# Optimization experiments

Measured on AMD Instinct MI355X. Metric: run time of the kernel, lower is better.

The kernel has to match this reference:

```python
import jax, jax.numpy as jnp
import numpy as np

B, A, D, H = 2048, 16, 128, 512

def setup_inputs() -> dict:
    key = jax.random.key(0)
    k0, k1, k2, k3, k4 = jax.random.split(key, 5)
    s1 = 1.0 / np.sqrt(D)
    s2 = 1.0 / np.sqrt(H)
    return {
        "attribute_embeddings": jax.random.normal(k0, (B, A, D), dtype=jnp.float32),
        "W1": jax.random.uniform(k1, (H, D), jnp.float32, -s1, s1),  # torch Linear weight [out,in]
        "b1": jax.random.uniform(k2, (H,), jnp.float32, -s1, s1),
        "W2": jax.random.uniform(k3, (D, H), jnp.float32, -s2, s2),
        "b2": jax.random.uniform(k4, (D,), jnp.float32, -s2, s2),
    }

def reference(attribute_embeddings, W1, b1, W2, b2):
    x = attribute_embeddings  # [B, A, D]
    # all pairwise elementwise products: [B, A, A, D]
    pairs = x[:, :, None, :] * x[:, None, :, :]
    # shared 2-layer MLP applied to every pair (torch Linear: y = x @ W.T + b)
    h = jax.nn.relu(jnp.einsum("bijd,hd->bijh", pairs, W1) + b1)
    inter = jnp.einsum("bijh,dh->bijd", h, W2) + b2  # [B, A, A, D]
    # sum over first attribute index i -> [B, A, D]
    return jnp.sum(inter, axis=1)
```

## Files before the change

kernel.cpp:

```cpp
#include <hip/hip_runtime.h>


#define BATCH 2048
#define AA 16
#define DD 128
#define HH 512

typedef __bf16 bf16;
typedef bf16  bf16x4 __attribute__((ext_vector_type(4)));
typedef bf16  bf16x8 __attribute__((ext_vector_type(8)));
typedef float f32x4  __attribute__((ext_vector_type(4)));

__device__ inline f32x4 splat4(float v) { f32x4 r = {v, v, v, v}; return r; }

__global__ __launch_bounds__(256, 1)
void convert_weights(const float* __restrict__ W1,
                     const float* __restrict__ W2,
                     bf16* __restrict__ wsb)
{
    int t = blockIdx.x * 256 + threadIdx.x;
    f32x4 v = (t < 16384) ? *(const f32x4*)(W1 + 4 * t)
                          : *(const f32x4*)(W2 + 4 * (t - 16384));
    bf16x4 o;
    o[0] = (bf16)v[0]; o[1] = (bf16)v[1]; o[2] = (bf16)v[2]; o[3] = (bf16)v[3];
    *(bf16x4*)(wsb + 4 * t) = o;
}

__global__ __launch_bounds__(512, 4)
void interact_kernel(const float* __restrict__ x,
                     const bf16*  __restrict__ W1b,
                     const float* __restrict__ b1,
                     const bf16*  __restrict__ W2b,
                     const float* __restrict__ b2,
                     float* __restrict__ out)
{
    __shared__ float xs[16][136];
    __shared__ __align__(16) unsigned char smem_raw[16 * 16 * 136 * 2];
    bf16 (*ps)[16][136] = reinterpret_cast<bf16(*)[16][136]>(smem_raw);
    bf16 (*hs)[520]     = reinterpret_cast<bf16(*)[520]>(smem_raw);

    const int b    = blockIdx.x;
    const int tid  = threadIdx.x;
    const int wave = tid >> 6;
    const int lane = tid & 63;
    const int quad = lane >> 4;
    const int col  = lane & 15;

    const int jrow = tid >> 5;
    const int dq   = (tid & 31) * 4;

    f32x4 xj;
    {
        const float* src = x + (size_t)b * (AA * DD) + jrow * DD + dq;
        xj = *(const f32x4*)src;
        *(f32x4*)(&xs[jrow][dq]) = xj;
    }

    bf16x8 w1f[4][4];
    f32x4  bias4[4];
#pragma unroll
    for (int n = 0; n < 4; ++n) {
        int h   = wave * 64 + n * 16 + col;
        bias4[n] = splat4(b1[h]);
#pragma unroll
        for (int kk = 0; kk < 4; ++kk)
            w1f[n][kk] = *(const bf16x8*)(W1b + h * DD + kk * 32 + quad * 8);
    }

    f32x4 hsum[4];
#pragma unroll
    for (int n = 0; n < 4; ++n) hsum[n] = splat4(0.f);

    __syncthreads();

#pragma unroll 4
    for (int i = 0; i < 16; ++i) {
        f32x4 xi = *(f32x4*)(&xs[i][dq]);
        bf16x4 pr;
#pragma unroll
        for (int e = 0; e < 4; ++e) pr[e] = (bf16)(xj[e] * xi[e]);
        *(bf16x4*)(&ps[i][jrow][dq]) = pr;
    }
    __syncthreads();

    const int i0 = wave * 2;
#pragma unroll 1
    for (int t = 0; t < 16; ++t) {
        const int i = (i0 + t) & 15;

        bf16x8 af[4];
#pragma unroll
        for (int kk = 0; kk < 4; ++kk)
            af[kk] = *(bf16x8*)(&ps[i][col][kk * 32 + quad * 8]);

        __builtin_amdgcn_s_setprio(1);
        f32x4 acc[4];
#pragma unroll
        for (int n = 0; n < 4; ++n)
            acc[n] = __builtin_amdgcn_mfma_f32_16x16x32_bf16(
                af[0], w1f[n][0], bias4[n], 0, 0, 0);
#pragma unroll
        for (int kk = 1; kk < 4; ++kk)
#pragma unroll
            for (int n = 0; n < 4; ++n)
                acc[n] = __builtin_amdgcn_mfma_f32_16x16x32_bf16(
                    af[kk], w1f[n][kk], acc[n], 0, 0, 0);
        __builtin_amdgcn_s_setprio(0);

#pragma unroll
        for (int n = 0; n < 4; ++n)
#pragma unroll
            for (int r = 0; r < 4; ++r)
                hsum[n][r] += fmaxf(acc[n][r], 0.f);
    }

    __syncthreads();

#pragma unroll
    for (int n = 0; n < 4; ++n)
#pragma unroll
        for (int r = 0; r < 4; ++r)
            hs[quad * 4 + r][wave * 64 + n * 16 + col] = (bf16)hsum[n][r];

    __syncthreads();

    const int d = wave * 16 + col;
    f32x4 acc2 = splat4(16.f * b2[d]);

#pragma unroll
    for (int ks = 0; ks < 16; ++ks) {
        int h0 = ks * 32 + quad * 8;
        bf16x8 a2 = *(bf16x8*)(&hs[col][h0]);
        bf16x8 bw = *(const bf16x8*)(W2b + d * HH + h0);
        acc2 = __builtin_amdgcn_mfma_f32_16x16x32_bf16(a2, bw, acc2, 0, 0, 0);
    }

#pragma unroll
    for (int r = 0; r < 4; ++r) {
        int j = quad * 4 + r;
        out[(size_t)b * (AA * DD) + j * DD + d] = acc2[r];
    }
}

extern "C" void kernel_launch(void* const* d_in, const int* in_sizes, int n_in,
                              void* d_out, int out_size, void* d_ws, size_t ws_size,
                              hipStream_t stream)
{
    const float* x  = (const float*)d_in[0];
    const float* W1 = (const float*)d_in[1];
    const float* b1 = (const float*)d_in[2];
    const float* W2 = (const float*)d_in[3];
    const float* b2 = (const float*)d_in[4];
    float* out = (float*)d_out;

    bf16* wsb = (bf16*)d_ws;
    convert_weights<<<128, 256, 0, stream>>>(W1, W2, wsb);

    const bf16* W1b = wsb;
    const bf16* W2b = wsb + (size_t)HH * DD;
    interact_kernel<<<BATCH, 512, 0, stream>>>(x, W1b, b1, W2b, b2, out);
}
```

Measured before the change: 153.4 us.

## Exploit pair symmetry to compute only half of pairwise MLP first layer

Uses the symmetry x_i*x_j = x_j*x_i to evaluate the first MLP layer for only 9 cyclic offsets instead of all 16 rows. Mirrored contributions are recovered by cross-lane ds_bpermute from the same tile. This shrinks the shared pair buffer and removes wave priority hints. It trades roughly 44% fewer first-layer MFMAs for extra permute and add instructions and a fully unrolled loop that raises register pressure.

```diff
diff --git a/kernel.cpp b/kernel.cpp
--- a/kernel.cpp
+++ b/kernel.cpp
@@ -12,6 +12,10 @@
 typedef float f32x4  __attribute__((ext_vector_type(4)));
 
 __device__ inline f32x4 splat4(float v) { f32x4 r = {v, v, v, v}; return r; }
+
+__device__ inline float bperm_f32(int idx, float v) {
+    return __int_as_float(__builtin_amdgcn_ds_bpermute(idx, __float_as_int(v)));
+}
 
 __global__ __launch_bounds__(256, 1)
 void convert_weights(const float* __restrict__ W1,
@@ -35,7 +39,7 @@
                      float* __restrict__ out)
 {
     __shared__ float xs[16][136];
-    __shared__ __align__(16) unsigned char smem_raw[16 * 16 * 136 * 2];
+    __shared__ __align__(16) unsigned char smem_raw[9 * 16 * 136 * 2];
     bf16 (*ps)[16][136] = reinterpret_cast<bf16(*)[16][136]>(smem_raw);
     bf16 (*hs)[520]     = reinterpret_cast<bf16(*)[520]>(smem_raw);
 
@@ -60,7 +64,7 @@
     f32x4  bias4[4];
 #pragma unroll
     for (int n = 0; n < 4; ++n) {
-        int h   = wave * 64 + n * 16 + col;
+        int h    = wave * 64 + n * 16 + col;
         bias4[n] = splat4(b1[h]);
 #pragma unroll
         for (int kk = 0; kk < 4; ++kk)
@@ -73,27 +77,26 @@
 
     __syncthreads();
 
-#pragma unroll 4
-    for (int i = 0; i < 16; ++i) {
-        f32x4 xi = *(f32x4*)(&xs[i][dq]);
+#pragma unroll
+    for (int dlt = 0; dlt < 9; ++dlt) {
+        f32x4 xi = *(f32x4*)(&xs[(jrow + dlt) & 15][dq]);
         bf16x4 pr;
 #pragma unroll
         for (int e = 0; e < 4; ++e) pr[e] = (bf16)(xj[e] * xi[e]);
-        *(bf16x4*)(&ps[i][jrow][dq]) = pr;
+        *(bf16x4*)(&ps[dlt][jrow][dq]) = pr;
     }
     __syncthreads();
 
-    const int i0 = wave * 2;
-#pragma unroll 1
-    for (int t = 0; t < 16; ++t) {
-        const int i = (i0 + t) & 15;
+    const int col4 = col << 2;
+    const int qrow = quad << 2;
 
+#pragma unroll
+    for (int dlt = 0; dlt < 9; ++dlt) {
         bf16x8 af[4];
 #pragma unroll
         for (int kk = 0; kk < 4; ++kk)
-            af[kk] = *(bf16x8*)(&ps[i][col][kk * 32 + quad * 8]);
+            af[kk] = *(bf16x8*)(&ps[dlt][col][kk * 32 + quad * 8]);
 
-        __builtin_amdgcn_s_setprio(1);
         f32x4 acc[4];
 #pragma unroll
         for (int n = 0; n < 4; ++n)
@@ -105,13 +108,33 @@
             for (int n = 0; n < 4; ++n)
                 acc[n] = __builtin_amdgcn_mfma_f32_16x16x32_bf16(
                     af[kk], w1f[n][kk], acc[n], 0, 0, 0);
-        __builtin_amdgcn_s_setprio(0);
 
 #pragma unroll
         for (int n = 0; n < 4; ++n)
 #pragma unroll
             for (int r = 0; r < 4; ++r)
-                hsum[n][r] += fmaxf(acc[n][r], 0.f);
+                acc[n][r] = fmaxf(acc[n][r], 0.f);
+
+        if (dlt >= 1 && dlt <= 7) {
+            int idx[4];
+#pragma unroll
+            for (int r = 0; r < 4; ++r) {
+                int srow = (qrow + r - dlt) & 15;
+                idx[r] = ((srow >> 2) << 6) | col4;
+            }
+#pragma unroll
+            for (int n = 0; n < 4; ++n)
+#pragma unroll
+                for (int r = 0; r < 4; ++r)
+                    hsum[n][r] += acc[n][r] +
+                                  bperm_f32(idx[r], acc[n][(r - dlt) & 3]);
+        } else {
+#pragma unroll
+            for (int n = 0; n < 4; ++n)
+#pragma unroll
+                for (int r = 0; r < 4; ++r)
+                    hsum[n][r] += acc[n][r];
+        }
     }
 
     __syncthreads();
```

New measurement: 525.1 us. 242% more time.
